# Kernel tuning notes

Hardware: AMD Instinct MI355X
Metric: run time of the kernel (lower is better)

The kernel has to match this reference:

```python
import jax, jax.numpy as jnp
import numpy as np

K_REP = 4          # repulsion neighbors
REP_THRESH = 0.02  # repulsion distance threshold
K_NORM = 16        # PCA-normal neighborhood size (includes self)
CD_W, REP_W, NORM_W = 1.0, 0.1, 0.01


def _pdist2(x, y):
    # squared pairwise distances: [B,N,M]
    xx = (x * x).sum(-1)
    yy = (y * y).sum(-1)
    return xx[..., :, None] + yy[..., None, :] - 2.0 * jnp.einsum('bnd,bmd->bnm', x, y)


def _gather_points(pts, idx):
    # pts: [B,N,3], idx: [B,N,k] -> [B,N,k,3]
    return jax.vmap(lambda p, i: p[i])(pts, idx)


def _pca_normals(pts):
    # normals via PCA over K_NORM nearest neighbors (self included)
    D = _pdist2(pts, pts)                       # [B,N,N]
    _, idx = jax.lax.top_k(-D, K_NORM)          # [B,N,K]
    nb = _gather_points(pts, idx)               # [B,N,K,3]
    c = nb - nb.mean(axis=-2, keepdims=True)
    cov = jnp.einsum('bnkd,bnke->bnde', c, c) / K_NORM  # [B,N,3,3]
    _, vecs = jnp.linalg.eigh(cov)              # ascending eigenvalues
    return vecs[..., :, 0]                      # eigenvector of smallest eigenvalue


def reference(pred, gt):
    # --- chamfer distance (squared, bidirectional mean) ---
    Dpg = _pdist2(pred, gt)                     # [B,N,M]
    cd = Dpg.min(axis=-1).mean() + Dpg.min(axis=-2).mean()

    # --- repulsion loss: k=4 NN on pred (excluding self) ---
    Dpp = _pdist2(pred, pred)                   # [B,N,N]
    neg_d2, _ = jax.lax.top_k(-Dpp, K_REP + 1)  # nearest incl. self
    d2 = -neg_d2[..., 1:]                       # drop self
    d = jnp.sqrt(jnp.maximum(d2, 1e-12))
    rep = jax.nn.relu(REP_THRESH - d).mean()

    # --- normal consistency via PCA normals (k=16) ---
    n_pred = _pca_normals(pred)
    n_gt = _pca_normals(gt)
    normc = 1.0 - (n_pred * n_gt).sum(-1).mean()

    return CD_W * cd + REP_W * rep + NORM_W * normc


def setup_inputs() -> dict:
    key = jax.random.key(0)
    k1, k2 = jax.random.split(key)
    B, N = 8, 2048
    pred = jax.random.uniform(k1, (B, N, 3), dtype=jnp.float32)
    gt = jax.random.uniform(k2, (B, N, 3), dtype=jnp.float32)
    return {"pred": pred, "gt": gt}
```

## Files before the change

kernel.cpp:

```cpp
#include <hip/hip_runtime.h>


#define NB 8
#define NP 2048
#define KW 10
#define KN 16


__device__ __forceinline__ float f_slapy2(float x, float y) {
    float xa = fabsf(x), ya = fabsf(y);
    float w = fmaxf(xa, ya), zm = fminf(xa, ya);
    if (zm == 0.f) return w;
    float q = zm / w;
    return w * sqrtf(1.f + q * q);
}

__device__ __forceinline__ void f_slartg(float f, float g, float* cs, float* sn, float* r) {
    if (g == 0.f) { *cs = 1.f; *sn = 0.f; *r = f; }
    else if (f == 0.f) { *cs = 0.f; *sn = copysignf(1.f, g); *r = fabsf(g); }
    else {
        float d = sqrtf(__fadd_rn(__fmul_rn(f, f), __fmul_rn(g, g)));
        *cs = fabsf(f) / d;
        *r  = copysignf(d, f);
        *sn = g / *r;
    }
}

__device__ void f_slaev2(float a, float b, float c,
                         float* rt1, float* rt2, float* cs1, float* sn1) {
    float sm = a + c;
    float df = a - c;
    float adf = fabsf(df);
    float tb = b + b;
    float ab = fabsf(tb);
    float acmx, acmn;
    if (fabsf(a) > fabsf(c)) { acmx = a; acmn = c; } else { acmx = c; acmn = a; }
    float rt;
    if (adf > ab)      { float q = ab / adf; rt = adf * sqrtf(1.f + q * q); }
    else if (adf < ab) { float q = adf / ab; rt = ab * sqrtf(1.f + q * q); }
    else               rt = ab * sqrtf(2.f);
    int sgn1;
    if (sm < 0.f) {
        *rt1 = 0.5f * (sm - rt); sgn1 = -1;
        *rt2 = (acmx / *rt1) * acmn - (b / *rt1) * b;
    } else if (sm > 0.f) {
        *rt1 = 0.5f * (sm + rt); sgn1 = 1;
        *rt2 = (acmx / *rt1) * acmn - (b / *rt1) * b;
    } else {
        *rt1 = 0.5f * rt; *rt2 = -0.5f * rt; sgn1 = 1;
    }
    float cs; int sgn2;
    if (df >= 0.f) { cs = df + rt; sgn2 = 1; }
    else           { cs = df - rt; sgn2 = -1; }
    float acs = fabsf(cs);
    if (acs > ab) {
        float ct = -tb / cs;
        *sn1 = 1.f / sqrtf(1.f + ct * ct);
        *cs1 = ct * *sn1;
    } else {
        if (ab == 0.f) { *cs1 = 1.f; *sn1 = 0.f; }
        else {
            float tn = -cs / tb;
            *cs1 = 1.f / sqrtf(1.f + tn * tn);
            *sn1 = tn * *cs1;
        }
    }
    if (sgn1 == sgn2) { float tn = *cs1; *cs1 = -*sn1; *sn1 = tn; }
}

__device__ void ssyevd3_evec0(float a00, float a10, float a20,
                              float a11, float a21, float a22,
                              float* ox, float* oy, float* oz) {
    float d[3], e[2];
    float tau = 0.f, v2 = 0.f;
    float xnorm = fabsf(a20);
    if (xnorm == 0.f) {
        tau = 0.f;
        d[0] = a00; d[1] = a11; d[2] = a22; e[0] = a10; e[1] = a21;
    } else {
        float beta = -copysignf(f_slapy2(a10, xnorm), a10);
        tau = (beta - a10) / beta;
        float inv = 1.f / (a10 - beta);
        v2 = a20 * inv;
        float x1 = tau * (a11 + a21 * v2);
        float x2 = tau * (a21 + a22 * v2);
        float alpha = -0.5f * tau * (x1 + x2 * v2);
        float w1 = x1 + alpha;
        float w2 = x2 + alpha * v2;
        float b11 = a11 - 2.f * w1;
        float b21 = a21 - v2 * w1 - w2;
        float b22 = a22 - 2.f * (v2 * w2);
        d[0] = a00; d[1] = b11; d[2] = b22; e[0] = beta; e[1] = b21;
    }
    const float eps    = 5.9604645e-08f;
    const float eps2   = eps * eps;
    const float safmin = 1.1754944e-38f;
    const float ssfmax = sqrtf(1.f / safmin) / 3.f;
    const float ssfmin = sqrtf(safmin) / eps2;
    const int n = 3, nmaxit = 90;
    float z[3][3] = {{1.f,0.f,0.f},{0.f,1.f,0.f},{0.f,0.f,1.f}};
    int jtot = 0;
    int l1 = 1;

    while (true) {
        if (l1 > n) break;
        if (l1 > 1) e[l1 - 2] = 0.f;
        int m = n;
        for (int mi = l1; mi <= n - 1; ++mi) {
            float tst = fabsf(e[mi - 1]);
            if (tst == 0.f) { m = mi; break; }
            if (tst <= (sqrtf(fabsf(d[mi - 1])) * sqrtf(fabsf(d[mi]))) * eps) {
                e[mi - 1] = 0.f; m = mi; break;
            }
        }
        int l = l1, lsv = l, lend = m, lendsv = lend;
        l1 = m + 1;
        if (lend == l) continue;

        float anorm = 0.f;
        for (int i = l; i <= lend; ++i) anorm = fmaxf(anorm, fabsf(d[i - 1]));
        for (int i = l; i <= lend - 1; ++i) anorm = fmaxf(anorm, fabsf(e[i - 1]));
        int iscale = 0; float sclto = 1.f;
        if (anorm == 0.f) continue;
        if (anorm > ssfmax) { iscale = 1; sclto = ssfmax; }
        else if (anorm < ssfmin) { iscale = 2; sclto = ssfmin; }
        if (iscale) {
            float mul = sclto / anorm;
            for (int i = l; i <= lend; ++i) d[i - 1] *= mul;
            for (int i = l; i <= lend - 1; ++i) e[i - 1] *= mul;
        }
        if (fabsf(d[lend - 1]) < fabsf(d[l - 1])) { lend = lsv; l = lendsv; }

        if (lend > l) {
            while (true) {
                int mq = lend;
                if (l != lend) {
                    for (int i = l; i <= lend - 1; ++i) {
                        float ei = e[i - 1];
                        float tst = ei * ei;
                        if (tst <= (eps2 * fabsf(d[i - 1])) * fabsf(d[i]) + safmin) { mq = i; break; }
                    }
                }
                if (mq < lend) e[mq - 1] = 0.f;
                float p = d[l - 1];
                if (mq == l) { d[l - 1] = p; l = l + 1; if (l <= lend) continue; break; }
                if (mq == l + 1) {
                    float rt1, rt2, c, s;
                    f_slaev2(d[l - 1], e[l - 1], d[l], &rt1, &rt2, &c, &s);
                    for (int i = 0; i < 3; ++i) {
                        float temp = z[i][l];
                        z[i][l]     = c * temp - s * z[i][l - 1];
                        z[i][l - 1] = s * temp + c * z[i][l - 1];
                    }
                    d[l - 1] = rt1; d[l] = rt2; e[l - 1] = 0.f;
                    l += 2; if (l <= lend) continue; break;
                }
                if (jtot == nmaxit) break;
                jtot++;
                float g = (d[l] - p) / (2.f * e[l - 1]);
                float r = f_slapy2(g, 1.f);
                g = d[mq - 1] - p + e[l - 1] / (g + copysignf(r, g));
                float s = 1.f, c = 1.f; p = 0.f;
                float cw[2], sw[2];
                for (int i = mq - 1; i >= l; --i) {
                    float f = s * e[i - 1];
                    float b = c * e[i - 1];
                    f_slartg(g, f, &c, &s, &r);
                    if (i != mq - 1) e[i] = r;
                    g = d[i] - p;
                    r = (d[i - 1] - g) * s + 2.f * c * b;
                    p = s * r;
                    d[i] = g + p;
                    g = c * r - b;
                    cw[i - l] = c; sw[i - l] = -s;
                }
                for (int j = mq - l; j >= 1; --j) {
                    float cj = cw[j - 1], sj = sw[j - 1];
                    int c0 = l - 1 + (j - 1);
                    for (int i = 0; i < 3; ++i) {
                        float temp = z[i][c0 + 1];
                        z[i][c0 + 1] = cj * temp - sj * z[i][c0];
                        z[i][c0]     = sj * temp + cj * z[i][c0];
                    }
                }
                d[l - 1] -= p;
                e[l - 1] = g;
            }
        } else {
            while (true) {
                int mq = lend;
                if (l != lend) {
                    for (int i = l; i >= lend + 1; --i) {
                        float ei = e[i - 2];
                        float tst = ei * ei;
                        if (tst <= (eps2 * fabsf(d[i - 1])) * fabsf(d[i - 2]) + safmin) { mq = i; break; }
                    }
                }
                if (mq > lend) e[mq - 2] = 0.f;
                float p = d[l - 1];
                if (mq == l) { d[l - 1] = p; l = l - 1; if (l >= lend) continue; break; }
                if (mq == l - 1) {
                    float rt1, rt2, c, s;
                    f_slaev2(d[l - 2], e[l - 2], d[l - 1], &rt1, &rt2, &c, &s);
                    for (int i = 0; i < 3; ++i) {
                        float temp = z[i][l - 1];
                        z[i][l - 1] = c * temp - s * z[i][l - 2];
                        z[i][l - 2] = s * temp + c * z[i][l - 2];
                    }
                    d[l - 2] = rt1; d[l - 1] = rt2; e[l - 2] = 0.f;
                    l -= 2; if (l >= lend) continue; break;
                }
                if (jtot == nmaxit) break;
                jtot++;
                float g = (d[l - 2] - p) / (2.f * e[l - 2]);
                float r = f_slapy2(g, 1.f);
                g = d[mq - 1] - p + e[l - 2] / (g + copysignf(r, g));
                float s = 1.f, c = 1.f; p = 0.f;
                float cw[2], sw[2];
                for (int i = mq; i <= l - 1; ++i) {
                    float f = s * e[i - 1];
                    float b = c * e[i - 1];
                    f_slartg(g, f, &c, &s, &r);
                    if (i != mq) e[i - 2] = r;
                    g = d[i - 1] - p;
                    r = (d[i] - g) * s + 2.f * c * b;
                    p = s * r;
                    d[i - 1] = g + p;
                    g = c * r - b;
                    cw[i - mq] = c; sw[i - mq] = s;
                }
                for (int j = 1; j <= l - mq; ++j) {
                    float cj = cw[j - 1], sj = sw[j - 1];
                    int c0 = mq - 1 + (j - 1);
                    for (int i = 0; i < 3; ++i) {
                        float temp = z[i][c0 + 1];
                        z[i][c0 + 1] = cj * temp - sj * z[i][c0];
                        z[i][c0]     = sj * temp + cj * z[i][c0];
                    }
                }
                d[l - 1] -= p;
                e[l - 2] = g;
            }
        }
        if (iscale) {
            float mul = anorm / sclto;
            for (int i = lsv; i <= lendsv; ++i) d[i - 1] *= mul;
            for (int i = lsv; i <= lendsv - 1; ++i) e[i - 1] *= mul;
        }
        if (jtot >= nmaxit) break;
    }

    for (int ii = 2; ii <= 3; ++ii) {
        int i = ii - 1, k = i;
        float p = d[i - 1];
        for (int j = ii; j <= 3; ++j) if (d[j - 1] < p) { k = j; p = d[j - 1]; }
        if (k != i) {
            d[k - 1] = d[i - 1]; d[i - 1] = p;
            for (int r = 0; r < 3; ++r) { float t = z[r][i - 1]; z[r][i - 1] = z[r][k - 1]; z[r][k - 1] = t; }
        }
    }
    float r0 = z[0][0], r1 = z[1][0], r2 = z[2][0];
    if (tau != 0.f) {
        float sum = r1 + v2 * r2;
        r1 -= tau * sum;
        r2 -= tau * (v2 * sum);
    }
    *ox = r0; *oy = r1; *oz = r2;
}


__device__ __forceinline__ float dot_rn(float ax, float ay, float az,
                                        float bx, float by, float bz) {
    return __fadd_rn(__fadd_rn(__fmul_rn(ax, bx), __fmul_rn(ay, by)), __fmul_rn(az, bz));
}

__device__ __forceinline__ void chain10(unsigned k[KW], unsigned x) {
    unsigned t = x;
    #pragma unroll
    for (int s = 0; s < KW; ++s) {
        unsigned lo = k[s] < t ? k[s] : t;
        unsigned hi = k[s] < t ? t : k[s];
        k[s] = lo; t = hi;
    }
}
__device__ __forceinline__ void chain16(unsigned k[KN], unsigned x) {
    unsigned t = x;
    #pragma unroll
    for (int s = 0; s < KN; ++s) {
        unsigned lo = k[s] < t ? k[s] : t;
        unsigned hi = k[s] < t ? t : k[s];
        k[s] = lo; t = hi;
    }
}

#define KIDX(s, w, l) (((s) * 8 + (w)) * 64 + (l))

__global__ __launch_bounds__(512) void scan_kernel(
    const float* __restrict__ pred, const float* __restrict__ gt,
    float* __restrict__ nP, float* __restrict__ nG, double* __restrict__ acc)
{
    __shared__ float4 sHome[NP];
    __shared__ float4 sOther[NP];
    unsigned* kbuf = (unsigned*)sOther;
    float* mbuf = (float*)((char*)sOther + 20480);
    float* cache = (float*)sOther;

    int bi = blockIdx.x;
    bool predHome = bi < NB * 32;
    int lb = predHome ? bi : bi - NB * 32;
    int b = lb >> 5;
    int tile = lb & 31;
    int tid  = threadIdx.x;
    int wave = tid >> 6;
    int lane = tid & 63;

    const float* home  = (predHome ? pred : gt) + (size_t)b * NP * 3;
    const float* other = (predHome ? gt : pred) + (size_t)b * NP * 3;

    for (int t = tid; t < NP; t += 512) {
        float hx = home[3 * t], hy = home[3 * t + 1], hz = home[3 * t + 2];
        sHome[t] = make_float4(hx, hy, hz, dot_rn(hx, hy, hz, hx, hy, hz));
        float ox = other[3 * t], oy = other[3 * t + 1], oz = other[3 * t + 2];
        sOther[t] = make_float4(ox, oy, oz, 0.f);
    }
    __syncthreads();

    int im = tile * 64 + lane;
    float4 q = sHome[im];
    float qx = q.x, qy = q.y, qz = q.z, qq = q.w;

    unsigned keys[KW];
    #pragma unroll
    for (int s = 0; s < KW; ++s) keys[s] = 0x7F800000u | (unsigned)s;

    float minv = 1e30f;

    for (int t = 0; t < NP / 8; ++t) {
        int jj = (t << 3) | wave;
        float4 h = sHome[jj];
        float dotj = dot_rn(qx, qy, qz, h.x, h.y, h.z);
        float d2 = __fsub_rn(__fadd_rn(qq, h.w), __fmul_rn(2.f, dotj));
        chain10(keys, (__float_as_uint(d2) & 0xFFFFF800u) | (unsigned)jj);
        float4 o = sOther[jj];
        float ex = qx - o.x, ey = qy - o.y, ez = qz - o.z;
        minv = fminf(minv, fmaf(ex, ex, fmaf(ey, ey, ez * ez)));
    }
    __syncthreads();

    #pragma unroll
    for (int s = 0; s < KW; ++s) kbuf[KIDX(s, wave, lane)] = keys[s];
    mbuf[wave * 64 + lane] = minv;
    __syncthreads();

    if (wave != 0) return;

    unsigned k16[KN];
    #pragma unroll
    for (int s = 0; s < KW; ++s) k16[s] = keys[s];
    #pragma unroll
    for (int s = KW; s < KN; ++s) k16[s] = 0x7F800000u | (unsigned)s;
    for (int w = 1; w < 8; ++w) {
        #pragma unroll
        for (int s = 0; s < KW; ++s) chain16(k16, kbuf[KIDX(s, w, lane)]);
    }
    minv = fminf(fminf(fminf(mbuf[lane], mbuf[64 + lane]),
                       fminf(mbuf[128 + lane], mbuf[192 + lane])),
                 fminf(fminf(mbuf[256 + lane], mbuf[320 + lane]),
                       fminf(mbuf[384 + lane], mbuf[448 + lane])));

    unsigned flags = 0;
    #pragma unroll
    for (int w = 0; w < 8; ++w)
        flags |= (kbuf[KIDX(KW - 1, w, lane)] < k16[15]) ? (1u << w) : 0u;

    if (__any(flags != 0)) {
        #pragma unroll
        for (int s = 0; s < KN; ++s)
            k16[s] = flags ? (0x7F800000u | (unsigned)s) : k16[s];
        for (int w = 0; w < 8; ++w) {
            #pragma unroll
            for (int s = 0; s < KW; ++s) {
                unsigned kk = kbuf[KIDX(s, w, lane)];
                bool use = (flags != 0) && !((flags >> w) & 1);
                chain16(k16, use ? kk : 0xFFFFFFFFu);
            }
        }
        for (int w = 0; w < 8; ++w) {
            if (__any((flags >> w) & 1)) {
                bool actw = ((flags >> w) & 1) != 0;
                for (int t = 0; t < NP / 8; ++t) {
                    int jj = (t << 3) | w;
                    float4 h = sHome[jj];
                    float dotj = dot_rn(qx, qy, qz, h.x, h.y, h.z);
                    float d2 = __fsub_rn(__fadd_rn(qq, h.w), __fmul_rn(2.f, dotj));
                    unsigned key = (__float_as_uint(d2) & 0xFFFFF800u) | (unsigned)jj;
                    chain16(k16, actw ? key : 0xFFFFFFFFu);
                }
            }
        }
    }

    float rep = 0.0f;
    if (predHome) {
        #pragma unroll
        for (int r = 1; r <= 4; ++r) {
            float d2 = __uint_as_float(k16[r] & 0xFFFFF800u);
            float dd = sqrtf(fmaxf(d2, 1e-12f));
            rep += fmaxf(0.02f - dd, 0.0f);
        }
    }

    float sx = 0.f, sy = 0.f, sz = 0.f;
    #pragma unroll
    for (int s = 0; s < KN; ++s) {
        const float* hp = home + 3 * (size_t)(k16[s] & 0x7FFu);
        float px = hp[0], py = hp[1], pz = hp[2];
        cache[(s * 3 + 0) * 64 + lane] = px;
        cache[(s * 3 + 1) * 64 + lane] = py;
        cache[(s * 3 + 2) * 64 + lane] = pz;
        sx += px; sy += py; sz += pz;
    }
    float mx = sx * (1.0f / KN), my = sy * (1.0f / KN), mz = sz * (1.0f / KN);
    float cxx = 0.f, cxy = 0.f, cxz = 0.f, cyy = 0.f, cyz = 0.f, czz = 0.f;
    #pragma unroll
    for (int s = 0; s < KN; ++s) {
        float ax = cache[(s * 3 + 0) * 64 + lane] - mx;
        float ay = cache[(s * 3 + 1) * 64 + lane] - my;
        float az = cache[(s * 3 + 2) * 64 + lane] - mz;
        cxx += ax * ax; cxy += ax * ay; cxz += ax * az;
        cyy += ay * ay; cyz += ay * az; czz += az * az;
    }
    cxx *= (1.f / KN); cxy *= (1.f / KN); cxz *= (1.f / KN);
    cyy *= (1.f / KN); cyz *= (1.f / KN); czz *= (1.f / KN);

    float nx, ny, nz;
    ssyevd3_evec0(cxx, cxy, cxz, cyy, cyz, czz, &nx, &ny, &nz);

    float* nout = predHome ? nP : nG;
    int gi = b * NP + im;
    nout[gi * 3 + 0] = nx;
    nout[gi * 3 + 1] = ny;
    nout[gi * 3 + 2] = nz;

    double part = (double)minv * (1.0 / (NB * NP))
                + (double)rep  * (0.1 / (NB * NP * 4));

    #pragma unroll
    for (int off = 32; off > 0; off >>= 1) part += __shfl_down(part, off);
    if (lane == 0) atomicAdd(acc, part);
}

__global__ __launch_bounds__(1024) void dotfin_kernel(
    const float* __restrict__ nP, const float* __restrict__ nG,
    const double* __restrict__ acc, float* __restrict__ out)
{
    int tid = threadIdx.x;
    float s = 0.f;
    for (int i = tid; i < NB * NP; i += 1024)
        s += nP[3 * i] * nG[3 * i] + nP[3 * i + 1] * nG[3 * i + 1] + nP[3 * i + 2] * nG[3 * i + 2];
    double part = (double)s;
    #pragma unroll
    for (int off = 32; off > 0; off >>= 1) part += __shfl_down(part, off);
    __shared__ double w[16];
    if ((tid & 63) == 0) w[tid >> 6] = part;
    __syncthreads();
    if (tid == 0) {
        double t = 0.0;
        for (int k = 0; k < 16; ++k) t += w[k];
        out[0] = (float)(acc[0] - t * (0.01 / (NB * NP)) + 0.01);
    }
}

extern "C" void kernel_launch(void* const* d_in, const int* in_sizes, int n_in,
                              void* d_out, int out_size, void* d_ws, size_t ws_size,
                              hipStream_t stream)
{
    const float* pred = (const float*)d_in[0];
    const float* gt   = (const float*)d_in[1];

    char* base = (char*)d_ws;
    double* acc = (double*)base;
    float* nP = (float*)(base + 64);
    float* nG = nP + (size_t)NB * NP * 3;

    hipMemsetAsync(d_ws, 0, 64, stream);
    scan_kernel<<<dim3(NB * 32 * 2), dim3(512), 0, stream>>>(pred, gt, nP, nG, acc);
    dotfin_kernel<<<dim3(1), dim3(1024), 0, stream>>>(nP, nG, acc, (float*)d_out);
}
```

Before: 171.3 us.

## Scalarize eigen-solver arrays into registers, raise occupancy, split final reduction

Replaces the small d/e/z arrays in the 3x3 tridiagonal QL eigen-solver with individual scalar variables, using select-based get/set macros and fully unrolled predicated loops. The aim is to keep them out of scratch memory, where dynamic indexing would otherwise place them. It also adds a min-blocks hint of 4 to the scan kernel's launch bounds, capping register use to raise occupancy. The single-block dot/finalize kernel becomes a 16-block atomic dot kernel plus a one-thread finalize kernel, at the cost of an extra launch and an added double atomic.

```diff
diff --git a/kernel.cpp b/kernel.cpp
--- a/kernel.cpp
+++ b/kernel.cpp
@@ -68,15 +68,40 @@
     if (sgn1 == sgn2) { float tn = *cs1; *cs1 = -*sn1; *sn1 = tn; }
 }
 
+
+__device__ __forceinline__ float get3(float a, float b, float c, int i) {
+    return i == 0 ? a : (i == 1 ? b : c);
+}
+__device__ __forceinline__ void set3(float& a, float& b, float& c, int i, float v) {
+    a = (i == 0) ? v : a;
+    b = (i == 1) ? v : b;
+    c = (i == 2) ? v : c;
+}
+__device__ __forceinline__ float get2(float a, float b, int i) { return i == 0 ? a : b; }
+__device__ __forceinline__ void set2(float& a, float& b, int i, float v) {
+    a = (i == 0) ? v : a;
+    b = (i == 1) ? v : b;
+}
+
+#define DGET(i)    get3(dd0, dd1, dd2, (i))
+#define DSET(i, v) set3(dd0, dd1, dd2, (i), (v))
+#define EGET(i)    get2(ee0, ee1, (i))
+#define ESET(i, v) set2(ee0, ee1, (i), (v))
+#define ZGET(r, c)    get3(z##r##0, z##r##1, z##r##2, (c))
+#define ZSET(r, c, v) set3(z##r##0, z##r##1, z##r##2, (c), (v))
+#define ZROT(r, ca, cb, cc, ss) { float zt_ = ZGET(r, (ca)); float zb_ = ZGET(r, (cb)); \
+    ZSET(r, (ca), (cc) * zt_ - (ss) * zb_); ZSET(r, (cb), (ss) * zt_ + (cc) * zb_); }
+#define ZROT3(ca, cb, cc, ss) { ZROT(0, (ca), (cb), (cc), (ss)) ZROT(1, (ca), (cb), (cc), (ss)) ZROT(2, (ca), (cb), (cc), (ss)) }
+
 __device__ void ssyevd3_evec0(float a00, float a10, float a20,
                               float a11, float a21, float a22,
                               float* ox, float* oy, float* oz) {
-    float d[3], e[2];
+    float dd0, dd1, dd2, ee0, ee1;
     float tau = 0.f, v2 = 0.f;
     float xnorm = fabsf(a20);
     if (xnorm == 0.f) {
         tau = 0.f;
-        d[0] = a00; d[1] = a11; d[2] = a22; e[0] = a10; e[1] = a21;
+        dd0 = a00; dd1 = a11; dd2 = a22; ee0 = a10; ee1 = a21;
     } else {
         float beta = -copysignf(f_slapy2(a10, xnorm), a10);
         tau = (beta - a10) / beta;
@@ -90,7 +115,7 @@
         float b11 = a11 - 2.f * w1;
         float b21 = a21 - v2 * w1 - w2;
         float b22 = a22 - 2.f * (v2 * w2);
-        d[0] = a00; d[1] = b11; d[2] = b22; e[0] = beta; e[1] = b21;
+        dd0 = a00; dd1 = b11; dd2 = b22; ee0 = beta; ee1 = b21;
     }
     const float eps    = 5.9604645e-08f;
     const float eps2   = eps * eps;
@@ -98,19 +123,27 @@
     const float ssfmax = sqrtf(1.f / safmin) / 3.f;
     const float ssfmin = sqrtf(safmin) / eps2;
     const int n = 3, nmaxit = 90;
-    float z[3][3] = {{1.f,0.f,0.f},{0.f,1.f,0.f},{0.f,0.f,1.f}};
+    float z00 = 1.f, z01 = 0.f, z02 = 0.f;
+    float z10 = 0.f, z11 = 1.f, z12 = 0.f;
+    float z20 = 0.f, z21 = 0.f, z22 = 1.f;
     int jtot = 0;
     int l1 = 1;
 
     while (true) {
         if (l1 > n) break;
-        if (l1 > 1) e[l1 - 2] = 0.f;
+        if (l1 > 1) ESET(l1 - 2, 0.f);
         int m = n;
-        for (int mi = l1; mi <= n - 1; ++mi) {
-            float tst = fabsf(e[mi - 1]);
-            if (tst == 0.f) { m = mi; break; }
-            if (tst <= (sqrtf(fabsf(d[mi - 1])) * sqrtf(fabsf(d[mi]))) * eps) {
-                e[mi - 1] = 0.f; m = mi; break;
+        {
+            bool found = false;
+            #pragma unroll
+            for (int mi = 1; mi <= 2; ++mi) {
+                if (!found && mi >= l1) {
+                    float tst = fabsf(EGET(mi - 1));
+                    if (tst == 0.f) { m = mi; found = true; }
+                    else if (tst <= (sqrtf(fabsf(DGET(mi - 1))) * sqrtf(fabsf(DGET(mi)))) * eps) {
+                        ESET(mi - 1, 0.f); m = mi; found = true;
+                    }
+                }
             }
         }
         int l = l1, lsv = l, lend = m, lendsv = lend;
@@ -118,148 +151,171 @@
         if (lend == l) continue;
 
         float anorm = 0.f;
-        for (int i = l; i <= lend; ++i) anorm = fmaxf(anorm, fabsf(d[i - 1]));
-        for (int i = l; i <= lend - 1; ++i) anorm = fmaxf(anorm, fabsf(e[i - 1]));
+        #pragma unroll
+        for (int i = 1; i <= 3; ++i)
+            if (i >= l && i <= lend) anorm = fmaxf(anorm, fabsf(DGET(i - 1)));
+        #pragma unroll
+        for (int i = 1; i <= 2; ++i)
+            if (i >= l && i <= lend - 1) anorm = fmaxf(anorm, fabsf(EGET(i - 1)));
         int iscale = 0; float sclto = 1.f;
         if (anorm == 0.f) continue;
         if (anorm > ssfmax) { iscale = 1; sclto = ssfmax; }
         else if (anorm < ssfmin) { iscale = 2; sclto = ssfmin; }
         if (iscale) {
             float mul = sclto / anorm;
-            for (int i = l; i <= lend; ++i) d[i - 1] *= mul;
-            for (int i = l; i <= lend - 1; ++i) e[i - 1] *= mul;
-        }
-        if (fabsf(d[lend - 1]) < fabsf(d[l - 1])) { lend = lsv; l = lendsv; }
+            #pragma unroll
+            for (int i = 1; i <= 3; ++i)
+                if (i >= l && i <= lend) DSET(i - 1, DGET(i - 1) * mul);
+            #pragma unroll
+            for (int i = 1; i <= 2; ++i)
+                if (i >= l && i <= lend - 1) ESET(i - 1, EGET(i - 1) * mul);
+        }
+        if (fabsf(DGET(lend - 1)) < fabsf(DGET(l - 1))) { lend = lsv; l = lendsv; }
 
         if (lend > l) {
             while (true) {
                 int mq = lend;
                 if (l != lend) {
-                    for (int i = l; i <= lend - 1; ++i) {
-                        float ei = e[i - 1];
-                        float tst = ei * ei;
-                        if (tst <= (eps2 * fabsf(d[i - 1])) * fabsf(d[i]) + safmin) { mq = i; break; }
-                    }
-                }
-                if (mq < lend) e[mq - 1] = 0.f;
-                float p = d[l - 1];
-                if (mq == l) { d[l - 1] = p; l = l + 1; if (l <= lend) continue; break; }
+                    bool found = false;
+                    #pragma unroll
+                    for (int i = 1; i <= 2; ++i) {
+                        if (!found && i >= l && i <= lend - 1) {
+                            float ei = EGET(i - 1);
+                            float tst = ei * ei;
+                            if (tst <= (eps2 * fabsf(DGET(i - 1))) * fabsf(DGET(i)) + safmin) { mq = i; found = true; }
+                        }
+                    }
+                }
+                if (mq < lend) ESET(mq - 1, 0.f);
+                float p = DGET(l - 1);
+                if (mq == l) { DSET(l - 1, p); l = l + 1; if (l <= lend) continue; break; }
                 if (mq == l + 1) {
                     float rt1, rt2, c, s;
-                    f_slaev2(d[l - 1], e[l - 1], d[l], &rt1, &rt2, &c, &s);
-                    for (int i = 0; i < 3; ++i) {
-                        float temp = z[i][l];
-                        z[i][l]     = c * temp - s * z[i][l - 1];
-                        z[i][l - 1] = s * temp + c * z[i][l - 1];
-                    }
-                    d[l - 1] = rt1; d[l] = rt2; e[l - 1] = 0.f;
+                    f_slaev2(DGET(l - 1), EGET(l - 1), DGET(l), &rt1, &rt2, &c, &s);
+                    ZROT3(l, l - 1, c, s);
+                    DSET(l - 1, rt1); DSET(l, rt2); ESET(l - 1, 0.f);
                     l += 2; if (l <= lend) continue; break;
                 }
                 if (jtot == nmaxit) break;
                 jtot++;
-                float g = (d[l] - p) / (2.f * e[l - 1]);
+                float g = (DGET(l) - p) / (2.f * EGET(l - 1));
                 float r = f_slapy2(g, 1.f);
-                g = d[mq - 1] - p + e[l - 1] / (g + copysignf(r, g));
+                g = DGET(mq - 1) - p + EGET(l - 1) / (g + copysignf(r, g));
                 float s = 1.f, c = 1.f; p = 0.f;
-                float cw[2], sw[2];
-                for (int i = mq - 1; i >= l; --i) {
-                    float f = s * e[i - 1];
-                    float b = c * e[i - 1];
-                    f_slartg(g, f, &c, &s, &r);
-                    if (i != mq - 1) e[i] = r;
-                    g = d[i] - p;
-                    r = (d[i - 1] - g) * s + 2.f * c * b;
-                    p = s * r;
-                    d[i] = g + p;
-                    g = c * r - b;
-                    cw[i - l] = c; sw[i - l] = -s;
-                }
-                for (int j = mq - l; j >= 1; --j) {
-                    float cj = cw[j - 1], sj = sw[j - 1];
-                    int c0 = l - 1 + (j - 1);
-                    for (int i = 0; i < 3; ++i) {
-                        float temp = z[i][c0 + 1];
-                        z[i][c0 + 1] = cj * temp - sj * z[i][c0];
-                        z[i][c0]     = sj * temp + cj * z[i][c0];
-                    }
-                }
-                d[l - 1] -= p;
-                e[l - 1] = g;
+                float cw0 = 0.f, cw1 = 0.f, sw0 = 0.f, sw1 = 0.f;
+                #pragma unroll
+                for (int i = 2; i >= 1; --i) {
+                    if (i <= mq - 1 && i >= l) {
+                        float f = s * EGET(i - 1);
+                        float b = c * EGET(i - 1);
+                        f_slartg(g, f, &c, &s, &r);
+                        if (i != mq - 1) ESET(i, r);
+                        g = DGET(i) - p;
+                        r = (DGET(i - 1) - g) * s + 2.f * c * b;
+                        p = s * r;
+                        DSET(i, g + p);
+                        g = c * r - b;
+                        set2(cw0, cw1, i - l, c);
+                        set2(sw0, sw1, i - l, -s);
+                    }
+                }
+                #pragma unroll
+                for (int j = 2; j >= 1; --j) {
+                    if (j <= mq - l) {
+                        float cj = get2(cw0, cw1, j - 1), sj = get2(sw0, sw1, j - 1);
+                        int c0 = l - 1 + (j - 1);
+                        ZROT3(c0 + 1, c0, cj, sj);
+                    }
+                }
+                DSET(l - 1, DGET(l - 1) - p);
+                ESET(l - 1, g);
             }
         } else {
             while (true) {
                 int mq = lend;
                 if (l != lend) {
-                    for (int i = l; i >= lend + 1; --i) {
-                        float ei = e[i - 2];
-                        float tst = ei * ei;
-                        if (tst <= (eps2 * fabsf(d[i - 1])) * fabsf(d[i - 2]) + safmin) { mq = i; break; }
-                    }
-                }
-                if (mq > lend) e[mq - 2] = 0.f;
-                float p = d[l - 1];
-                if (mq == l) { d[l - 1] = p; l = l - 1; if (l >= lend) continue; break; }
+                    bool found = false;
+                    #pragma unroll
+                    for (int i = 3; i >= 2; --i) {
+                        if (!found && i <= l && i >= lend + 1) {
+                            float ei = EGET(i - 2);
+                            float tst = ei * ei;
+                            if (tst <= (eps2 * fabsf(DGET(i - 1))) * fabsf(DGET(i - 2)) + safmin) { mq = i; found = true; }
+                        }
+                    }
+                }
+                if (mq > lend) ESET(mq - 2, 0.f);
+                float p = DGET(l - 1);
+                if (mq == l) { DSET(l - 1, p); l = l - 1; if (l >= lend) continue; break; }
                 if (mq == l - 1) {
                     float rt1, rt2, c, s;
-                    f_slaev2(d[l - 2], e[l - 2], d[l - 1], &rt1, &rt2, &c, &s);
-                    for (int i = 0; i < 3; ++i) {
-                        float temp = z[i][l - 1];
-                        z[i][l - 1] = c * temp - s * z[i][l - 2];
-                        z[i][l - 2] = s * temp + c * z[i][l - 2];
-                    }
-                    d[l - 2] = rt1; d[l - 1] = rt2; e[l - 2] = 0.f;
+                    f_slaev2(DGET(l - 2), EGET(l - 2), DGET(l - 1), &rt1, &rt2, &c, &s);
+                    ZROT3(l - 1, l - 2, c, s);
+                    DSET(l - 2, rt1); DSET(l - 1, rt2); ESET(l - 2, 0.f);
                     l -= 2; if (l >= lend) continue; break;
                 }
                 if (jtot == nmaxit) break;
                 jtot++;
-                float g = (d[l - 2] - p) / (2.f * e[l - 2]);
+                float g = (DGET(l - 2) - p) / (2.f * EGET(l - 2));
                 float r = f_slapy2(g, 1.f);
-                g = d[mq - 1] - p + e[l - 2] / (g + copysignf(r, g));
+                g = DGET(mq - 1) - p + EGET(l - 2) / (g + copysignf(r, g));
                 float s = 1.f, c = 1.f; p = 0.f;
-                float cw[2], sw[2];
-                for (int i = mq; i <= l - 1; ++i) {
-                    float f = s * e[i - 1];
-                    float b = c * e[i - 1];
-                    f_slartg(g, f, &c, &s, &r);
-                    if (i != mq) e[i - 2] = r;
-                    g = d[i - 1] - p;
-                    r = (d[i] - g) * s + 2.f * c * b;
-                    p = s * r;
-                    d[i - 1] = g + p;
-                    g = c * r - b;
-                    cw[i - mq] = c; sw[i - mq] = s;
-                }
-                for (int j = 1; j <= l - mq; ++j) {
-                    float cj = cw[j - 1], sj = sw[j - 1];
-                    int c0 = mq - 1 + (j - 1);
-                    for (int i = 0; i < 3; ++i) {
-                        float temp = z[i][c0 + 1];
-                        z[i][c0 + 1] = cj * temp - sj * z[i][c0];
-                        z[i][c0]     = sj * temp + cj * z[i][c0];
-                    }
-                }
-                d[l - 1] -= p;
-                e[l - 2] = g;
+                float cw0 = 0.f, cw1 = 0.f, sw0 = 0.f, sw1 = 0.f;
+                #pragma unroll
+                for (int i = 1; i <= 2; ++i) {
+                    if (i >= mq && i <= l - 1) {
+                        float f = s * EGET(i - 1);
+                        float b = c * EGET(i - 1);
+                        f_slartg(g, f, &c, &s, &r);
+                        if (i != mq) ESET(i - 2, r);
+                        g = DGET(i - 1) - p;
+                        r = (DGET(i) - g) * s + 2.f * c * b;
+                        p = s * r;
+                        DSET(i - 1, g + p);
+                        g = c * r - b;
+                        set2(cw0, cw1, i - mq, c);
+                        set2(sw0, sw1, i - mq, s);
+                    }
+                }
+                #pragma unroll
+                for (int j = 1; j <= 2; ++j) {
+                    if (j <= l - mq) {
+                        float cj = get2(cw0, cw1, j - 1), sj = get2(sw0, sw1, j - 1);
+                        int c0 = mq - 1 + (j - 1);
+                        ZROT3(c0 + 1, c0, cj, sj);
+                    }
+                }
+                DSET(l - 1, DGET(l - 1) - p);
+                ESET(l - 2, g);
             }
         }
         if (iscale) {
             float mul = anorm / sclto;
-            for (int i = lsv; i <= lendsv; ++i) d[i - 1] *= mul;
-            for (int i = lsv; i <= lendsv - 1; ++i) e[i - 1] *= mul;
+            #pragma unroll
+            for (int i = 1; i <= 3; ++i)
+                if (i >= lsv && i <= lendsv) DSET(i - 1, DGET(i - 1) * mul);
+            #pragma unroll
+            for (int i = 1; i <= 2; ++i)
+                if (i >= lsv && i <= lendsv - 1) ESET(i - 1, EGET(i - 1) * mul);
         }
         if (jtot >= nmaxit) break;
     }
 
+    #pragma unroll
     for (int ii = 2; ii <= 3; ++ii) {
         int i = ii - 1, k = i;
-        float p = d[i - 1];
-        for (int j = ii; j <= 3; ++j) if (d[j - 1] < p) { k = j; p = d[j - 1]; }
+        float p = DGET(i - 1);
+        #pragma unroll
+        for (int j = ii; j <= 3; ++j)
+            if (DGET(j - 1) < p) { k = j; p = DGET(j - 1); }
         if (k != i) {
-            d[k - 1] = d[i - 1]; d[i - 1] = p;
-            for (int r = 0; r < 3; ++r) { float t = z[r][i - 1]; z[r][i - 1] = z[r][k - 1]; z[r][k - 1] = t; }
-        }
-    }
-    float r0 = z[0][0], r1 = z[1][0], r2 = z[2][0];
+            DSET(k - 1, DGET(i - 1)); DSET(i - 1, p);
+            { float t0 = ZGET(0, i - 1); ZSET(0, i - 1, ZGET(0, k - 1)); ZSET(0, k - 1, t0); }
+            { float t1 = ZGET(1, i - 1); ZSET(1, i - 1, ZGET(1, k - 1)); ZSET(1, k - 1, t1); }
+            { float t2 = ZGET(2, i - 1); ZSET(2, i - 1, ZGET(2, k - 1)); ZSET(2, k - 1, t2); }
+        }
+    }
+    float r0 = z00, r1 = z10, r2 = z20;
     if (tau != 0.f) {
         float sum = r1 + v2 * r2;
         r1 -= tau * sum;
@@ -295,7 +351,7 @@
 
 #define KIDX(s, w, l) (((s) * 8 + (w)) * 64 + (l))
 
-__global__ __launch_bounds__(512) void scan_kernel(
+__global__ __launch_bounds__(512, 4) void scan_kernel(
     const float* __restrict__ pred, const float* __restrict__ gt,
     float* __restrict__ nP, float* __restrict__ nG, double* __restrict__ acc)
 {
@@ -450,25 +506,23 @@
     if (lane == 0) atomicAdd(acc, part);
 }
 
-__global__ __launch_bounds__(1024) void dotfin_kernel(
+__global__ __launch_bounds__(64) void dot_kernel(
     const float* __restrict__ nP, const float* __restrict__ nG,
-    const double* __restrict__ acc, float* __restrict__ out)
+    double* __restrict__ acc)
 {
-    int tid = threadIdx.x;
+    int vt = blockIdx.x * 64 + threadIdx.x;
     float s = 0.f;
-    for (int i = tid; i < NB * NP; i += 1024)
+    for (int i = vt; i < NB * NP; i += 1024)
         s += nP[3 * i] * nG[3 * i] + nP[3 * i + 1] * nG[3 * i + 1] + nP[3 * i + 2] * nG[3 * i + 2];
     double part = (double)s;
     #pragma unroll
     for (int off = 32; off > 0; off >>= 1) part += __shfl_down(part, off);
-    __shared__ double w[16];
-    if ((tid & 63) == 0) w[tid >> 6] = part;
-    __syncthreads();
-    if (tid == 0) {
-        double t = 0.0;
-        for (int k = 0; k < 16; ++k) t += w[k];
-        out[0] = (float)(acc[0] - t * (0.01 / (NB * NP)) + 0.01);
-    }
+    if (threadIdx.x == 0) atomicAdd(acc + 1, part);
+}
+
+__global__ void fin_kernel(const double* __restrict__ acc, float* __restrict__ out)
+{
+    out[0] = (float)(acc[0] - acc[1] * (0.01 / (NB * NP)) + 0.01);
 }
 
 extern "C" void kernel_launch(void* const* d_in, const int* in_sizes, int n_in,
@@ -485,5 +539,6 @@
 
     hipMemsetAsync(d_ws, 0, 64, stream);
     scan_kernel<<<dim3(NB * 32 * 2), dim3(512), 0, stream>>>(pred, gt, nP, nG, acc);
-    dotfin_kernel<<<dim3(1), dim3(1024), 0, stream>>>(nP, nG, acc, (float*)d_out);
-}
+    dot_kernel<<<dim3(16), dim3(64), 0, stream>>>(nP, nG, acc);
+    fin_kernel<<<dim3(1), dim3(1), 0, stream>>>(acc, (float*)d_out);
+}
```

Result: faster. 164.8 us (-3.8%).
